# Kernel optimization log

Hardware: AMD Instinct MI355X
Metric: run time of the kernel (lower is better)

The kernel has to match this reference:

```python
import jax, jax.numpy as jnp
import numpy as np

VOCAB = 200000
P = 1000
B = 64
L = 2048

def setup_inputs() -> dict:
    key = jax.random.key(0)
    k1, k2, k3, k4, k5 = jax.random.split(key, 5)
    tokens = jax.random.randint(k1, (B, L), 0, VOCAB, dtype=jnp.int64)
    lengths = jax.random.randint(k2, (B,), 1, L + 1, dtype=jnp.int64)
    emb_table = jax.random.normal(k3, (VOCAB, P), dtype=jnp.float32)
    W = jax.random.normal(k4, (1, P), dtype=jnp.float32) / np.sqrt(P)
    b = jax.random.normal(k5, (1,), dtype=jnp.float32)
    return {"tokens": tokens, "lengths": lengths, "emb_table": emb_table, "W": W, "b": b}

def reference(tokens, lengths, emb_table, W, b):
    # Nested -> padded-with-zeros -> mean over dim=1 divides by max_len L
    # (torch.mean on the padded tensor), NOT per-sequence length.
    mask = (jnp.arange(L)[None, :] < lengths[:, None]).astype(emb_table.dtype)  # [B, L]
    emb = emb_table[tokens]                      # [B, L, P] gather
    pooled = jnp.einsum('blp,bl->bp', emb, mask) / jnp.asarray(L, emb_table.dtype)  # [B, P]
    logits = jax.nn.sigmoid(pooled @ W.T + b)    # [B, 1]
    return logits.reshape(B)
```

## Files before the change

### kernel.cpp

```cpp
#include <hip/hip_runtime.h>


constexpr int B_ = 64;
constexpr int L_ = 2048;
constexpr int P_ = 1000;
constexpr int CPS = 64;
constexpr int BDIM = 256;
constexpr int WAVES = BDIM / 64;

__global__ __launch_bounds__(BDIM) void pool_dot_kernel(
    const int* __restrict__ tokens,
    const int* __restrict__ lengths,
    const float* __restrict__ emb,
    const float* __restrict__ W,
    float* __restrict__ partial)
{
    const int blk   = blockIdx.x;
    const int seq   = blk >> 6;
    const int chunk = blk & (CPS - 1);
    const int lane  = threadIdx.x & 63;
    const int wave  = threadIdx.x >> 6;

    const int len = (int)lengths[seq];
    __shared__ float red[WAVES];

    float accl = 0.0f;
    const int t0 = chunk + 64 * wave;
    const int nm = (t0 < len) ? (((len - 1 - t0) >> 8) + 1) : 0;

    if (nm > 0) {
        const float4* W4 = (const float4*)W;
        float4 wf[4];
        #pragma unroll
        for (int k = 0; k < 4; ++k) {
            const int j = lane + 64 * k;
            if (j < P_ / 4) wf[k] = W4[j];
            else            wf[k] = make_float4(0.f, 0.f, 0.f, 0.f);
        }
        const int* trow = tokens + seq * L_;
        for (int m = 0; m < nm; ++m) {
            const int t   = t0 + (m << 8);
            const int row = trow[t];
            const float4* e4 = (const float4*)(emb + (size_t)row * P_);
            #pragma unroll
            for (int k = 0; k < 4; ++k) {
                const int j = lane + 64 * k;
                if (j < P_ / 4) {
                    const float4 e = e4[j];
                    accl = fmaf(e.x, wf[k].x, accl);
                    accl = fmaf(e.y, wf[k].y, accl);
                    accl = fmaf(e.z, wf[k].z, accl);
                    accl = fmaf(e.w, wf[k].w, accl);
                }
            }
        }
    }

    #pragma unroll
    for (int off = 32; off > 0; off >>= 1)
        accl += __shfl_down(accl, off, 64);
    if (lane == 0) red[wave] = accl;
    __syncthreads();
    if (threadIdx.x == 0) {
        float s = 0.0f;
        #pragma unroll
        for (int w = 0; w < WAVES; ++w) s += red[w];
        partial[blk] = s;
    }
}

__global__ void finalize_kernel(const float* __restrict__ partial,
                                const float* __restrict__ bias,
                                float* __restrict__ out)
{
    const int seq  = blockIdx.x;
    const int lane = threadIdx.x;
    float s = partial[seq * CPS + lane];
    #pragma unroll
    for (int off = 32; off > 0; off >>= 1)
        s += __shfl_down(s, off, 64);
    if (lane == 0) {
        const float v = s * (1.0f / (float)L_) + bias[0];
        out[seq] = 1.0f / (1.0f + expf(-v));
    }
}

extern "C" void kernel_launch(void* const* d_in, const int* in_sizes, int n_in,
                              void* d_out, int out_size, void* d_ws, size_t ws_size,
                              hipStream_t stream) {
    const int*   tokens  = (const int*)d_in[0];
    const int*   lengths = (const int*)d_in[1];
    const float* emb     = (const float*)d_in[2];
    const float* W       = (const float*)d_in[3];
    const float* bias    = (const float*)d_in[4];
    float* out     = (float*)d_out;
    float* partial = (float*)d_ws;

    pool_dot_kernel<<<B_ * CPS, BDIM, 0, stream>>>(tokens, lengths, emb, W, partial);
    finalize_kernel<<<B_, 64, 0, stream>>>(partial, bias, out);
}
```

Baseline: 48.36 us.

## Double chunks per sequence and collapse finalize into one block

Doubles the number of blocks per sequence, giving 8192 blocks, each covering tokens at a stride of 512, so per-wave token loops are shorter and more blocks are in flight for the latency-bound gather. It adds an unroll-4 hint on the token loop so several row loads can be issued together. The finalize kernel becomes a single 256-thread block in which four threads per sequence sum 32 partials each and combine them with xor shuffles. The cost is more block launches and scheduling overhead, plus less work per block, which weakens amortization of the W load.

```diff
diff --git a/kernel.cpp b/kernel.cpp
--- a/kernel.cpp
+++ b/kernel.cpp
@@ -4,9 +4,11 @@
 constexpr int B_ = 64;
 constexpr int L_ = 2048;
 constexpr int P_ = 1000;
-constexpr int CPS = 64;
+constexpr int CPS = 128;
 constexpr int BDIM = 256;
 constexpr int WAVES = BDIM / 64;
+constexpr int SLOTS = CPS * WAVES;
+constexpr int NBLK = B_ * CPS;
 
 __global__ __launch_bounds__(BDIM) void pool_dot_kernel(
     const int* __restrict__ tokens,
@@ -16,7 +18,7 @@
     float* __restrict__ partial)
 {
     const int blk   = blockIdx.x;
-    const int seq   = blk >> 6;
+    const int seq   = blk >> 7;
     const int chunk = blk & (CPS - 1);
     const int lane  = threadIdx.x & 63;
     const int wave  = threadIdx.x >> 6;
@@ -25,8 +27,8 @@
     __shared__ float red[WAVES];
 
     float accl = 0.0f;
-    const int t0 = chunk + 64 * wave;
-    const int nm = (t0 < len) ? (((len - 1 - t0) >> 8) + 1) : 0;
+    const int s0 = chunk + CPS * wave;
+    const int nm = (s0 < len) ? (((len - 1 - s0) >> 9) + 1) : 0;
 
     if (nm > 0) {
         const float4* W4 = (const float4*)W;
@@ -38,8 +40,9 @@
             else            wf[k] = make_float4(0.f, 0.f, 0.f, 0.f);
         }
         const int* trow = tokens + seq * L_;
+        #pragma unroll 4
         for (int m = 0; m < nm; ++m) {
-            const int t   = t0 + (m << 8);
+            const int t   = s0 + (m << 9);
             const int row = trow[t];
             const float4* e4 = (const float4*)(emb + (size_t)row * P_);
             #pragma unroll
@@ -69,17 +72,21 @@
     }
 }
 
-__global__ void finalize_kernel(const float* __restrict__ partial,
-                                const float* __restrict__ bias,
-                                float* __restrict__ out)
+__global__ __launch_bounds__(256) void finalize_kernel(
+    const float* __restrict__ partial,
+    const float* __restrict__ bias,
+    float* __restrict__ out)
 {
-    const int seq  = blockIdx.x;
-    const int lane = threadIdx.x;
-    float s = partial[seq * CPS + lane];
+    const int i   = threadIdx.x;
+    const int seq = i >> 2;
+    const int q   = i & 3;
+    float s = 0.0f;
     #pragma unroll
-    for (int off = 32; off > 0; off >>= 1)
-        s += __shfl_down(s, off, 64);
-    if (lane == 0) {
+    for (int j = 0; j < CPS / 4; ++j)
+        s += partial[seq * CPS + q + 4 * j];
+    s += __shfl_xor(s, 1, 64);
+    s += __shfl_xor(s, 2, 64);
+    if (q == 0) {
         const float v = s * (1.0f / (float)L_) + bias[0];
         out[seq] = 1.0f / (1.0f + expf(-v));
     }
@@ -96,6 +103,6 @@
     float* out     = (float*)d_out;
     float* partial = (float*)d_ws;
 
-    pool_dot_kernel<<<B_ * CPS, BDIM, 0, stream>>>(tokens, lengths, emb, W, partial);
-    finalize_kernel<<<B_, 64, 0, stream>>>(partial, bias, out);
+    pool_dot_kernel<<<NBLK, BDIM, 0, stream>>>(tokens, lengths, emb, W, partial);
+    finalize_kernel<<<1, 256, 0, stream>>>(partial, bias, out);
 }
```

Result: faster. 46.97 us (-2.9%).
